# Kernel optimization log

Measured on AMD Instinct MI355X. Metric: run time of the kernel, lower is better.

## Reference

```python
import jax, jax.numpy as jnp
import numpy as np

N_NODE, N_REL, EMB, N_NB, N_TYPES, B = 200000, 16, 128, 16, 4, 4096


def setup_inputs() -> dict:
    key = jax.random.key(0)
    ks = jax.random.split(key, 12)
    s = 1.0 / np.sqrt(EMB)
    return {
        "node": jax.random.randint(ks[0], (B,), 0, N_NODE),
        "relation": jax.random.randint(ks[1], (B,), 0, N_REL),
        "adj_node": jax.random.randint(ks[2], (N_NODE, N_NB), 0, N_NODE),
        "adj_rela": jax.random.randint(ks[3], (N_NODE, N_NB), 0, N_REL),
        "node_type": jax.random.randint(ks[4], (N_NODE,), 0, N_TYPES),
        "node_emb": jax.random.normal(ks[5], (N_NODE, EMB), jnp.float32) * s,
        "rela_emb": jax.random.normal(ks[6], (N_REL, EMB), jnp.float32) * s,
        "type_w": jax.random.uniform(ks[7], (N_TYPES, N_TYPES), jnp.float32),
        "Ws0": jax.random.normal(ks[8], (EMB, EMB), jnp.float32) * s,
        "Wn0": jax.random.normal(ks[9], (EMB, EMB), jnp.float32) * s,
        "Ws1": jax.random.normal(ks[10], (EMB, EMB), jnp.float32) * s,
        "Wn1": jax.random.normal(ks[11], (EMB, EMB), jnp.float32) * s,
    }


def _agg(self_v, nb_v, score, Ws, Wn):
    # self_v: [N,E], nb_v: [N,K,E], score: [N,K] (all neighbors valid -> no mask)
    w = jax.nn.softmax(score, axis=-1)
    agg = jnp.einsum("nk,nke->ne", w, nb_v)
    return self_v @ Ws + agg @ Wn


def reference(node, relation, adj_node, adj_rela, node_type, node_emb, rela_emb,
              type_w, Ws0, Wn0, Ws1, Wn1):
    # --- multi-hop neighbor expansion (get_neighbors) ---
    e1 = adj_node[node]                      # [B,16]
    r1 = adj_rela[node]                      # [B,16]
    e2 = adj_node[e1].reshape(B, -1)         # [B,256]
    r2 = adj_rela[e1].reshape(B, -1)         # [B,256]

    # --- prior embeddings with DistMult-style relation pre-transform ---
    rel_vec = rela_emb[relation]             # [B,E]
    ev0 = node_emb[node] * rel_vec                           # [B,E]
    ev1 = node_emb[e1] * rel_vec[:, None, :]                 # [B,16,E]
    ev2 = node_emb[e2] * rel_vec[:, None, :]                 # [B,256,E]

    # --- relation similarity |cosine| (calc_rsim) ---
    rn = rela_emb / jnp.maximum(jnp.linalg.norm(rela_emb, axis=-1, keepdims=True), 1e-8)
    rsim = jnp.abs(rn @ rn.T)                # [R,R]

    t0 = node_type[node]                     # [B]
    t1 = node_type[e1]                       # [B,16]
    t2 = node_type[e2]                       # [B,256]

    # --- iteration i=0, hop 0 ---
    score00 = rsim[relation[:, None], r1] * type_w[t0[:, None], t1]   # [B,16]
    v0 = jax.nn.relu(_agg(ev0, ev1, score00, Ws0, Wn0))               # [B,E]

    # --- iteration i=0, hop 1 ---
    self1 = ev1.reshape(B * N_NB, EMB)
    nb1 = ev2.reshape(B * N_NB, N_NB, EMB)
    tgt1 = jnp.repeat(relation, N_NB)
    score01 = (rsim[tgt1[:, None], r2.reshape(B * N_NB, N_NB)]
               * type_w[t1.reshape(-1)[:, None], t2.reshape(B * N_NB, N_NB)])
    v1 = jax.nn.relu(_agg(self1, nb1, score01, Ws0, Wn0)).reshape(B, N_NB, EMB)

    # --- iteration i=1, hop 0 (last: no activation) ---
    out = _agg(v0, v1, score00, Ws1, Wn1)    # [B,E]

    # post='none'; norm=1 -> L2 normalize
    out = out / jnp.maximum(jnp.linalg.norm(out, axis=-1, keepdims=True), 1e-12)
    return out
```

## Files before the change

### kernel.cpp

```cpp
#include <hip/hip_runtime.h>
#include <math.h>

#define NB   16
#define EMB  128
#define G    2
#define XSTRIDE 8704

typedef __bf16 bf16x8 __attribute__((ext_vector_type(8)));
typedef __bf16 bf16x4 __attribute__((ext_vector_type(4)));
typedef float  f32x4  __attribute__((ext_vector_type(4)));
typedef int    i32x4  __attribute__((ext_vector_type(4)));

__global__ __launch_bounds__(256) void pack_w_kernel(
    const float* __restrict__ Ws0, const float* __restrict__ Wn0,
    const float* __restrict__ Ws1, const float* __restrict__ Wn1,
    __bf16* __restrict__ pack)
{
    int idx = blockIdx.x * 256 + threadIdx.x;
    if (idx >= 8192) return;
    int l  = idx & 63;
    int nt = (idx >> 6) & 7;
    int s  = (idx >> 9) & 7;
    int m  = idx >> 12;
    int col = nt * 16 + (l & 15);
    int k0  = s * 32 + (l >> 4) * 8;
    const float* Wa = m ? Ws1 : Ws0;
    const float* Wb = m ? Wn1 : Wn0;
    bf16x8 v;
    #pragma unroll
    for (int j = 0; j < 8; ++j) {
        int k = k0 + j;
        float wv = (k < 128) ? Wa[k * EMB + col] : Wb[(k - 128) * EMB + col];
        v[j] = (__bf16)wv;
    }
    *(bf16x8*)(pack + (size_t)idx * 8) = v;
}

__global__ __launch_bounds__(256) void rsim_kernel(
    const float* __restrict__ rela_emb, float* __restrict__ rsim)
{
    __shared__ float dd[16][16];
    int t = threadIdx.x, r = t >> 4, c = t & 15;
    float d = 0.f;
    #pragma unroll
    for (int k4 = 0; k4 < 32; ++k4) {
        f32x4 a = *(const f32x4*)(rela_emb + r * EMB + k4 * 4);
        f32x4 b = *(const f32x4*)(rela_emb + c * EMB + k4 * 4);
        d += a[0]*b[0] + a[1]*b[1] + a[2]*b[2] + a[3]*b[3];
    }
    dd[r][c] = d;
    __syncthreads();
    float nr = fmaxf(sqrtf(dd[r][r]), 1e-8f);
    float nc = fmaxf(sqrtf(dd[c][c]), 1e-8f);
    rsim[t] = fabsf(d) / (nr * nc);
}

__global__ __launch_bounds__(256) void conv_emb_kernel(
    const float* __restrict__ src, __bf16* __restrict__ dst, int n4)
{
    int i = blockIdx.x * 256 + threadIdx.x;
    if (i >= n4) return;
    f32x4 v = ((const f32x4*)src)[i];
    bf16x4 o;
    o[0] = (__bf16)v[0]; o[1] = (__bf16)v[1];
    o[2] = (__bf16)v[2]; o[3] = (__bf16)v[3];
    ((bf16x4*)dst)[i] = o;
}

template<bool BT>
__device__ __forceinline__ f32x4 load_rq(const void* tab, int idx, int q) {
    if constexpr (BT) {
        bf16x4 v = *((const bf16x4*)tab + idx * 32 + q);
        f32x4 r;
        r[0] = (float)v[0]; r[1] = (float)v[1];
        r[2] = (float)v[2]; r[3] = (float)v[3];
        return r;
    } else {
        return *((const f32x4*)tab + idx * 32 + q);
    }
}

template<bool BT>
__global__ __launch_bounds__(256, 4) void gnn_kernel(
    const int* __restrict__ node, const int* __restrict__ relation,
    const int* __restrict__ adj_node, const int* __restrict__ adj_rela,
    const int* __restrict__ node_type, const void* __restrict__ tab,
    const float* __restrict__ rela_emb, const float* __restrict__ type_w,
    const __bf16* __restrict__ packW, const float* __restrict__ rsimg,
    float* __restrict__ out)
{
    __shared__ __align__(16) unsigned char Xb[G * XSTRIDE];
    __shared__ __align__(16) unsigned char Yb[16 * 512];
    __shared__ __align__(16) float scratch[1024];
    __shared__ __align__(16) float sw01[16][16];
    __shared__ __align__(16) int   se2[16][16];
    __shared__ __align__(16) float relv[EMB];
    __shared__ float sw00[G][16];
    __shared__ float srsim[16];
    __shared__ int   se1[16], sr1[16], st1[16];

    const int t  = threadIdx.x;
    const int b0 = blockIdx.x * G;

    {
        f32x4 z = {0.f, 0.f, 0.f, 0.f};
        *(f32x4*)(Yb + t * 16)        = z;
        *(f32x4*)(Yb + 4096 + t * 16) = z;
    }

    for (int e = 0; e < G; ++e) {
        const int nb0 = node[b0 + e];
        const int rel = relation[b0 + e];

        if (t < 16) {
            int e1 = adj_node[nb0 * NB + t];
            se1[t] = e1;
            sr1[t] = adj_rela[nb0 * NB + t];
            st1[t] = node_type[e1];
            srsim[t] = rsimg[rel * 16 + t];
        }
        if (t < EMB) relv[t] = rela_emb[rel * EMB + t];
        __syncthreads();

        {
            int k = t >> 4, j = t & 15;
            int e1k = se1[k];
            int e2  = adj_node[e1k * NB + j];
            int r2  = adj_rela[e1k * NB + j];
            int t2  = node_type[e2];
            se2[k][j] = e2;
            float s = srsim[r2] * type_w[st1[k] * 4 + t2];
            float m = s;
            #pragma unroll
            for (int off = 8; off >= 1; off >>= 1) m = fmaxf(m, __shfl_xor(m, off));
            float ex = __expf(s - m);
            float sum = ex;
            #pragma unroll
            for (int off = 8; off >= 1; off >>= 1) sum += __shfl_xor(sum, off);
            sw01[k][j] = ex / sum;
        }
        {
            int t0type = node_type[nb0];
            if (t < 16) {
                float s = srsim[sr1[t]] * type_w[t0type * 4 + st1[t]];
                float m = s;
                #pragma unroll
                for (int off = 8; off >= 1; off >>= 1) m = fmaxf(m, __shfl_xor(m, off));
                float ex = __expf(s - m);
                float sum = ex;
                #pragma unroll
                for (int off = 8; off >= 1; off >>= 1) sum += __shfl_xor(sum, off);
                sw00[e][t] = ex / sum;
            }
        }
        __syncthreads();

        unsigned char* Xe = Xb + e * XSTRIDE;
        {
            const int q = t & 31;
            const int g = t >> 5;
            const f32x4 rv4 = *(const f32x4*)&relv[q * 4];
            f32x4 pagg = {0.f, 0.f, 0.f, 0.f};

            for (int kx = 0; kx < 2; ++kx) {
                const int k = g + kx * 8;
                const int swz = (k & 7) << 4;

                const f32x4 sv = load_rq<BT>(tab, se1[k], q);
                pagg += sw00[e][k] * sv;
                bf16x4 xs;
                xs[0] = (__bf16)(sv[0] * rv4[0]);
                xs[1] = (__bf16)(sv[1] * rv4[1]);
                xs[2] = (__bf16)(sv[2] * rv4[2]);
                xs[3] = (__bf16)(sv[3] * rv4[3]);
                *(bf16x4*)(Xe + ((k * 512 + q * 8) ^ swz)) = xs;

                i32x4 i0 = *(const i32x4*)&se2[k][0];
                i32x4 i1 = *(const i32x4*)&se2[k][4];
                i32x4 i2 = *(const i32x4*)&se2[k][8];
                i32x4 i3 = *(const i32x4*)&se2[k][12];
                f32x4 w0 = *(const f32x4*)&sw01[k][0];
                f32x4 w1 = *(const f32x4*)&sw01[k][4];
                f32x4 w2 = *(const f32x4*)&sw01[k][8];
                f32x4 w3 = *(const f32x4*)&sw01[k][12];

                f32x4 v0  = load_rq<BT>(tab, i0[0], q);
                f32x4 v1  = load_rq<BT>(tab, i0[1], q);
                f32x4 v2  = load_rq<BT>(tab, i0[2], q);
                f32x4 v3  = load_rq<BT>(tab, i0[3], q);
                f32x4 v4  = load_rq<BT>(tab, i1[0], q);
                f32x4 v5  = load_rq<BT>(tab, i1[1], q);
                f32x4 v6  = load_rq<BT>(tab, i1[2], q);
                f32x4 v7  = load_rq<BT>(tab, i1[3], q);
                f32x4 v8  = load_rq<BT>(tab, i2[0], q);
                f32x4 v9  = load_rq<BT>(tab, i2[1], q);
                f32x4 v10 = load_rq<BT>(tab, i2[2], q);
                f32x4 v11 = load_rq<BT>(tab, i2[3], q);
                f32x4 v12 = load_rq<BT>(tab, i3[0], q);
                f32x4 v13 = load_rq<BT>(tab, i3[1], q);
                f32x4 v14 = load_rq<BT>(tab, i3[2], q);
                f32x4 v15 = load_rq<BT>(tab, i3[3], q);

                f32x4 s01 = w0[0] * v0;  s01 += w0[1] * v1;
                f32x4 s23 = w0[2] * v2;  s23 += w0[3] * v3;
                f32x4 s45 = w1[0] * v4;  s45 += w1[1] * v5;
                f32x4 s67 = w1[2] * v6;  s67 += w1[3] * v7;
                f32x4 s89 = w2[0] * v8;  s89 += w2[1] * v9;
                f32x4 sab = w2[2] * v10; sab += w2[3] * v11;
                f32x4 scd = w3[0] * v12; scd += w3[1] * v13;
                f32x4 sef = w3[2] * v14; sef += w3[3] * v15;
                s01 += s23; s45 += s67; s89 += sab; scd += sef;
                s01 += s45; s89 += scd;
                f32x4 acc = s01 + s89;

                bf16x4 xa;
                xa[0] = (__bf16)(acc[0] * rv4[0]);
                xa[1] = (__bf16)(acc[1] * rv4[1]);
                xa[2] = (__bf16)(acc[2] * rv4[2]);
                xa[3] = (__bf16)(acc[3] * rv4[3]);
                *(bf16x4*)(Xe + ((k * 512 + 256 + q * 8) ^ swz)) = xa;
            }
            ((f32x4*)scratch)[g * 32 + q] = pagg;
        }
        __syncthreads();
        if (t < 32) {
            f32x4 s = ((f32x4*)scratch)[t];
            #pragma unroll
            for (int g = 1; g < 8; ++g) s += ((f32x4*)scratch)[g * 32 + t];
            const f32x4 rv4 = *(const f32x4*)&relv[t * 4];
            const f32x4 ev0 = load_rq<BT>(tab, nb0, t);
            bf16x4 h0s, h0a;
            #pragma unroll
            for (int c = 0; c < 4; ++c) {
                h0s[c] = (__bf16)(ev0[c] * rv4[c]);
                h0a[c] = (__bf16)(s[c]   * rv4[c]);
            }
            *(bf16x4*)(Xe + 16 * 512 + t * 8)       = h0s;
            *(bf16x4*)(Xe + 16 * 512 + 256 + t * 8) = h0a;
        }
        __syncthreads();
    }

    const int w = t >> 6, l = t & 63;
    f32x4 acc[G][2][2];
    #pragma unroll
    for (int e = 0; e < G; ++e)
        #pragma unroll
        for (int m = 0; m < 2; ++m)
            #pragma unroll
            for (int n = 0; n < 2; ++n)
                acc[e][m][n] = (f32x4){0.f, 0.f, 0.f, 0.f};
    {
        const int row0 = l & 15;
        const int kb   = (l >> 4) * 16;
        const int sw0  = (row0 & 7) << 4;
        #pragma unroll
        for (int s = 0; s < 8; ++s) {
            bf16x8 bf0 = *(const bf16x8*)(packW + ((s * 8 + 2 * w) * 64 + l) * 8);
            bf16x8 bf1 = *(const bf16x8*)(packW + ((s * 8 + 2 * w + 1) * 64 + l) * 8);
            #pragma unroll
            for (int e = 0; e < G; ++e) {
                const unsigned char* Xe = Xb + e * XSTRIDE;
                bf16x8 a0 = *(const bf16x8*)(Xe + ((row0 * 512 + s * 64 + kb) ^ sw0));
                bf16x8 a1 = *(const bf16x8*)(Xe + (16 * 512 + s * 64 + kb));
                acc[e][0][0] = __builtin_amdgcn_mfma_f32_16x16x32_bf16(a0, bf0, acc[e][0][0], 0, 0, 0);
                acc[e][0][1] = __builtin_amdgcn_mfma_f32_16x16x32_bf16(a0, bf1, acc[e][0][1], 0, 0, 0);
                acc[e][1][0] = __builtin_amdgcn_mfma_f32_16x16x32_bf16(a1, bf0, acc[e][1][0], 0, 0, 0);
                acc[e][1][1] = __builtin_amdgcn_mfma_f32_16x16x32_bf16(a1, bf1, acc[e][1][1], 0, 0, 0);
            }
        }
    }

    #pragma unroll
    for (int e = 0; e < G; ++e) {
        const int rbase = (l >> 4) * 4;
        float s0 = 0.f, s1 = 0.f;
        #pragma unroll
        for (int r = 0; r < 4; ++r) {
            float wk = sw00[e][rbase + r];
            s0 = fmaf(wk, fmaxf(acc[e][0][0][r], 0.f), s0);
            s1 = fmaf(wk, fmaxf(acc[e][0][1][r], 0.f), s1);
        }
        s0 += __shfl_xor(s0, 16); s0 += __shfl_xor(s0, 32);
        s1 += __shfl_xor(s1, 16); s1 += __shfl_xor(s1, 32);
        if (l < 16) {
            int c0 = 2 * w * 16 + l, c1 = c0 + 16;
            const int swz = (e & 7) << 4;
            *(__bf16*)(Yb + ((e * 512 + c0 * 2) ^ swz))         = (__bf16)fmaxf(acc[e][1][0][0], 0.f);
            *(__bf16*)(Yb + ((e * 512 + c1 * 2) ^ swz))         = (__bf16)fmaxf(acc[e][1][1][0], 0.f);
            *(__bf16*)(Yb + ((e * 512 + (128 + c0) * 2) ^ swz)) = (__bf16)s0;
            *(__bf16*)(Yb + ((e * 512 + (128 + c1) * 2) ^ swz)) = (__bf16)s1;
        }
    }
    __syncthreads();

    {
        f32x4 h0 = {0.f, 0.f, 0.f, 0.f};
        f32x4 h1 = {0.f, 0.f, 0.f, 0.f};
        const int row0 = l & 15;
        const int kb   = (l >> 4) * 16;
        const int sw0  = (row0 & 7) << 4;
        const __bf16* packW1 = packW + 32768;
        #pragma unroll
        for (int s = 0; s < 8; ++s) {
            bf16x8 a   = *(const bf16x8*)(Yb + ((row0 * 512 + s * 64 + kb) ^ sw0));
            bf16x8 bf0 = *(const bf16x8*)(packW1 + ((s * 8 + 2 * w) * 64 + l) * 8);
            bf16x8 bf1 = *(const bf16x8*)(packW1 + ((s * 8 + 2 * w + 1) * 64 + l) * 8);
            h0 = __builtin_amdgcn_mfma_f32_16x16x32_bf16(a, bf0, h0, 0, 0, 0);
            h1 = __builtin_amdgcn_mfma_f32_16x16x32_bf16(a, bf1, h1, 0, 0, 0);
        }
        if (l < 16) {
            int c0 = 2 * w * 16 + l, c1 = c0 + 16;
            #pragma unroll
            for (int e = 0; e < G; ++e) {
                scratch[e * EMB + c0] = h0[e];
                scratch[e * EMB + c1] = h1[e];
            }
        }
    }
    __syncthreads();

    if (t < 64 * G) {
        int e  = t >> 6;
        int c2 = (t & 63) * 2;
        float a  = scratch[e * EMB + c2];
        float bb = scratch[e * EMB + c2 + 1];
        float sq = a * a + bb * bb;
        #pragma unroll
        for (int off = 1; off < 64; off <<= 1) sq += __shfl_xor(sq, off);
        float inv = 1.f / fmaxf(sqrtf(sq), 1e-12f);
        out[(b0 + e) * EMB + c2]     = a * inv;
        out[(b0 + e) * EMB + c2 + 1] = bb * inv;
    }
}

extern "C" void kernel_launch(void* const* d_in, const int* in_sizes, int n_in,
                              void* d_out, int out_size, void* d_ws, size_t ws_size,
                              hipStream_t stream) {
    (void)n_in; (void)out_size;
    const int*   node      = (const int*)d_in[0];
    const int*   relation  = (const int*)d_in[1];
    const int*   adj_node  = (const int*)d_in[2];
    const int*   adj_rela  = (const int*)d_in[3];
    const int*   node_type = (const int*)d_in[4];
    const float* node_emb  = (const float*)d_in[5];
    const float* rela_emb  = (const float*)d_in[6];
    const float* type_w    = (const float*)d_in[7];
    const float* Ws0       = (const float*)d_in[8];
    const float* Wn0       = (const float*)d_in[9];
    const float* Ws1       = (const float*)d_in[10];
    const float* Wn1       = (const float*)d_in[11];
    float* out = (float*)d_out;
    const int B     = in_sizes[0];
    const int nnode = in_sizes[5] / EMB;

    __bf16* packW = (__bf16*)d_ws;
    float*  rsimg = (float*)((char*)d_ws + 131072);
    __bf16* tabbf = (__bf16*)((char*)d_ws + 132096);
    const size_t need = 132096 + (size_t)nnode * EMB * 2;

    pack_w_kernel<<<32, 256, 0, stream>>>(Ws0, Wn0, Ws1, Wn1, packW);
    rsim_kernel<<<1, 256, 0, stream>>>(rela_emb, rsimg);

    const int grid = B / G;
    if (ws_size >= need) {
        const int n4 = nnode * EMB / 4;
        conv_emb_kernel<<<(n4 + 255) / 256, 256, 0, stream>>>(node_emb, tabbf, n4);
        gnn_kernel<true><<<grid, 256, 0, stream>>>(node, relation, adj_node, adj_rela,
                                                   node_type, (const void*)tabbf, rela_emb,
                                                   type_w, packW, rsimg, out);
    } else {
        gnn_kernel<false><<<grid, 256, 0, stream>>>(node, relation, adj_node, adj_rela,
                                                    node_type, (const void*)node_emb, rela_emb,
                                                    type_w, packW, rsimg, out);
    }
}
```

Baseline: 99.11 us.

## Process one batch element per block and reuse one LDS buffer across stages

Changes the gnn kernel from two batch elements per block (G=2) to one, launching B blocks. The Y buffer is dropped: the first-stage X buffer is zeroed and reused for the second-stage MFMA input, and scratch becomes a smaller shared array. The self-embedding row is written earlier by one warp. This cuts LDS use per block and accumulator registers, aiming for higher occupancy and more blocks to hide gather latency. In exchange, each B-fragment load of packW now feeds half as many MFMAs, and the kernel gains an extra barrier.

```diff
diff --git a/kernel.cpp b/kernel.cpp
--- a/kernel.cpp
+++ b/kernel.cpp
@@ -3,8 +3,6 @@
 
 #define NB   16
 #define EMB  128
-#define G    2
-#define XSTRIDE 8704
 
 typedef __bf16 bf16x8 __attribute__((ext_vector_type(8)));
 typedef __bf16 bf16x4 __attribute__((ext_vector_type(4)));
@@ -89,47 +87,51 @@
     const __bf16* __restrict__ packW, const float* __restrict__ rsimg,
     float* __restrict__ out)
 {
-    __shared__ __align__(16) unsigned char Xb[G * XSTRIDE];
-    __shared__ __align__(16) unsigned char Yb[16 * 512];
-    __shared__ __align__(16) float scratch[1024];
+    __shared__ __align__(16) unsigned char Xb[17 * 512];
+    __shared__ __align__(16) f32x4 scr4[8][32];
     __shared__ __align__(16) float sw01[16][16];
     __shared__ __align__(16) int   se2[16][16];
     __shared__ __align__(16) float relv[EMB];
-    __shared__ float sw00[G][16];
+    __shared__ float sw00[16];
     __shared__ float srsim[16];
     __shared__ int   se1[16], sr1[16], st1[16];
 
-    const int t  = threadIdx.x;
-    const int b0 = blockIdx.x * G;
-
-    {
-        f32x4 z = {0.f, 0.f, 0.f, 0.f};
-        *(f32x4*)(Yb + t * 16)        = z;
-        *(f32x4*)(Yb + 4096 + t * 16) = z;
-    }
-
-    for (int e = 0; e < G; ++e) {
-        const int nb0 = node[b0 + e];
-        const int rel = relation[b0 + e];
-
+    const int t   = threadIdx.x;
+    const int b   = blockIdx.x;
+    const int nb0 = node[b];
+    const int rel = relation[b];
+
+    if (t < 16) {
+        int e1 = adj_node[nb0 * NB + t];
+        se1[t] = e1;
+        sr1[t] = adj_rela[nb0 * NB + t];
+        st1[t] = node_type[e1];
+        srsim[t] = rsimg[rel * 16 + t];
+    }
+    if (t < EMB) relv[t] = rela_emb[rel * EMB + t];
+    __syncthreads();
+
+    {
+        int k = t >> 4, j = t & 15;
+        int e1k = se1[k];
+        int e2  = adj_node[e1k * NB + j];
+        int r2  = adj_rela[e1k * NB + j];
+        int t2  = node_type[e2];
+        se2[k][j] = e2;
+        float s = srsim[r2] * type_w[st1[k] * 4 + t2];
+        float m = s;
+        #pragma unroll
+        for (int off = 8; off >= 1; off >>= 1) m = fmaxf(m, __shfl_xor(m, off));
+        float ex = __expf(s - m);
+        float sum = ex;
+        #pragma unroll
+        for (int off = 8; off >= 1; off >>= 1) sum += __shfl_xor(sum, off);
+        sw01[k][j] = ex / sum;
+    }
+    {
+        int t0type = node_type[nb0];
         if (t < 16) {
-            int e1 = adj_node[nb0 * NB + t];
-            se1[t] = e1;
-            sr1[t] = adj_rela[nb0 * NB + t];
-            st1[t] = node_type[e1];
-            srsim[t] = rsimg[rel * 16 + t];
-        }
-        if (t < EMB) relv[t] = rela_emb[rel * EMB + t];
-        __syncthreads();
-
-        {
-            int k = t >> 4, j = t & 15;
-            int e1k = se1[k];
-            int e2  = adj_node[e1k * NB + j];
-            int r2  = adj_rela[e1k * NB + j];
-            int t2  = node_type[e2];
-            se2[k][j] = e2;
-            float s = srsim[r2] * type_w[st1[k] * 4 + t2];
+            float s = srsim[sr1[t]] * type_w[t0type * 4 + st1[t]];
             float m = s;
             #pragma unroll
             for (int off = 8; off >= 1; off >>= 1) m = fmaxf(m, __shfl_xor(m, off));
@@ -137,163 +139,150 @@
             float sum = ex;
             #pragma unroll
             for (int off = 8; off >= 1; off >>= 1) sum += __shfl_xor(sum, off);
-            sw01[k][j] = ex / sum;
-        }
-        {
-            int t0type = node_type[nb0];
-            if (t < 16) {
-                float s = srsim[sr1[t]] * type_w[t0type * 4 + st1[t]];
-                float m = s;
-                #pragma unroll
-                for (int off = 8; off >= 1; off >>= 1) m = fmaxf(m, __shfl_xor(m, off));
-                float ex = __expf(s - m);
-                float sum = ex;
-                #pragma unroll
-                for (int off = 8; off >= 1; off >>= 1) sum += __shfl_xor(sum, off);
-                sw00[e][t] = ex / sum;
-            }
-        }
-        __syncthreads();
-
-        unsigned char* Xe = Xb + e * XSTRIDE;
-        {
-            const int q = t & 31;
-            const int g = t >> 5;
-            const f32x4 rv4 = *(const f32x4*)&relv[q * 4];
-            f32x4 pagg = {0.f, 0.f, 0.f, 0.f};
-
-            for (int kx = 0; kx < 2; ++kx) {
-                const int k = g + kx * 8;
-                const int swz = (k & 7) << 4;
-
-                const f32x4 sv = load_rq<BT>(tab, se1[k], q);
-                pagg += sw00[e][k] * sv;
-                bf16x4 xs;
-                xs[0] = (__bf16)(sv[0] * rv4[0]);
-                xs[1] = (__bf16)(sv[1] * rv4[1]);
-                xs[2] = (__bf16)(sv[2] * rv4[2]);
-                xs[3] = (__bf16)(sv[3] * rv4[3]);
-                *(bf16x4*)(Xe + ((k * 512 + q * 8) ^ swz)) = xs;
-
-                i32x4 i0 = *(const i32x4*)&se2[k][0];
-                i32x4 i1 = *(const i32x4*)&se2[k][4];
-                i32x4 i2 = *(const i32x4*)&se2[k][8];
-                i32x4 i3 = *(const i32x4*)&se2[k][12];
-                f32x4 w0 = *(const f32x4*)&sw01[k][0];
-                f32x4 w1 = *(const f32x4*)&sw01[k][4];
-                f32x4 w2 = *(const f32x4*)&sw01[k][8];
-                f32x4 w3 = *(const f32x4*)&sw01[k][12];
-
-                f32x4 v0  = load_rq<BT>(tab, i0[0], q);
-                f32x4 v1  = load_rq<BT>(tab, i0[1], q);
-                f32x4 v2  = load_rq<BT>(tab, i0[2], q);
-                f32x4 v3  = load_rq<BT>(tab, i0[3], q);
-                f32x4 v4  = load_rq<BT>(tab, i1[0], q);
-                f32x4 v5  = load_rq<BT>(tab, i1[1], q);
-                f32x4 v6  = load_rq<BT>(tab, i1[2], q);
-                f32x4 v7  = load_rq<BT>(tab, i1[3], q);
-                f32x4 v8  = load_rq<BT>(tab, i2[0], q);
-                f32x4 v9  = load_rq<BT>(tab, i2[1], q);
-                f32x4 v10 = load_rq<BT>(tab, i2[2], q);
-                f32x4 v11 = load_rq<BT>(tab, i2[3], q);
-                f32x4 v12 = load_rq<BT>(tab, i3[0], q);
-                f32x4 v13 = load_rq<BT>(tab, i3[1], q);
-                f32x4 v14 = load_rq<BT>(tab, i3[2], q);
-                f32x4 v15 = load_rq<BT>(tab, i3[3], q);
-
-                f32x4 s01 = w0[0] * v0;  s01 += w0[1] * v1;
-                f32x4 s23 = w0[2] * v2;  s23 += w0[3] * v3;
-                f32x4 s45 = w1[0] * v4;  s45 += w1[1] * v5;
-                f32x4 s67 = w1[2] * v6;  s67 += w1[3] * v7;
-                f32x4 s89 = w2[0] * v8;  s89 += w2[1] * v9;
-                f32x4 sab = w2[2] * v10; sab += w2[3] * v11;
-                f32x4 scd = w3[0] * v12; scd += w3[1] * v13;
-                f32x4 sef = w3[2] * v14; sef += w3[3] * v15;
-                s01 += s23; s45 += s67; s89 += sab; scd += sef;
-                s01 += s45; s89 += scd;
-                f32x4 acc = s01 + s89;
-
-                bf16x4 xa;
-                xa[0] = (__bf16)(acc[0] * rv4[0]);
-                xa[1] = (__bf16)(acc[1] * rv4[1]);
-                xa[2] = (__bf16)(acc[2] * rv4[2]);
-                xa[3] = (__bf16)(acc[3] * rv4[3]);
-                *(bf16x4*)(Xe + ((k * 512 + 256 + q * 8) ^ swz)) = xa;
-            }
-            ((f32x4*)scratch)[g * 32 + q] = pagg;
-        }
-        __syncthreads();
-        if (t < 32) {
-            f32x4 s = ((f32x4*)scratch)[t];
+            sw00[t] = ex / sum;
+        }
+    }
+    __syncthreads();
+
+    {
+        const int q = t & 31;
+        const int g = t >> 5;
+        const f32x4 rv4 = *(const f32x4*)&relv[q * 4];
+        f32x4 pagg = {0.f, 0.f, 0.f, 0.f};
+
+        if (g == 0) {
+            const f32x4 ev0 = load_rq<BT>(tab, nb0, q);
+            bf16x4 h0s;
             #pragma unroll
-            for (int g = 1; g < 8; ++g) s += ((f32x4*)scratch)[g * 32 + t];
-            const f32x4 rv4 = *(const f32x4*)&relv[t * 4];
-            const f32x4 ev0 = load_rq<BT>(tab, nb0, t);
-            bf16x4 h0s, h0a;
-            #pragma unroll
-            for (int c = 0; c < 4; ++c) {
-                h0s[c] = (__bf16)(ev0[c] * rv4[c]);
-                h0a[c] = (__bf16)(s[c]   * rv4[c]);
-            }
-            *(bf16x4*)(Xe + 16 * 512 + t * 8)       = h0s;
-            *(bf16x4*)(Xe + 16 * 512 + 256 + t * 8) = h0a;
-        }
-        __syncthreads();
-    }
+            for (int c = 0; c < 4; ++c) h0s[c] = (__bf16)(ev0[c] * rv4[c]);
+            *(bf16x4*)(Xb + 16 * 512 + q * 8) = h0s;
+        }
+
+        for (int kx = 0; kx < 2; ++kx) {
+            const int k = g + kx * 8;
+            const int swz = (k & 7) << 4;
+
+            const f32x4 sv = load_rq<BT>(tab, se1[k], q);
+            pagg += sw00[k] * sv;
+            bf16x4 xs;
+            xs[0] = (__bf16)(sv[0] * rv4[0]);
+            xs[1] = (__bf16)(sv[1] * rv4[1]);
+            xs[2] = (__bf16)(sv[2] * rv4[2]);
+            xs[3] = (__bf16)(sv[3] * rv4[3]);
+            *(bf16x4*)(Xb + ((k * 512 + q * 8) ^ swz)) = xs;
+
+            i32x4 i0 = *(const i32x4*)&se2[k][0];
+            i32x4 i1 = *(const i32x4*)&se2[k][4];
+            i32x4 i2 = *(const i32x4*)&se2[k][8];
+            i32x4 i3 = *(const i32x4*)&se2[k][12];
+            f32x4 w0 = *(const f32x4*)&sw01[k][0];
+            f32x4 w1 = *(const f32x4*)&sw01[k][4];
+            f32x4 w2 = *(const f32x4*)&sw01[k][8];
+            f32x4 w3 = *(const f32x4*)&sw01[k][12];
+
+            f32x4 v0  = load_rq<BT>(tab, i0[0], q);
+            f32x4 v1  = load_rq<BT>(tab, i0[1], q);
+            f32x4 v2  = load_rq<BT>(tab, i0[2], q);
+            f32x4 v3  = load_rq<BT>(tab, i0[3], q);
+            f32x4 v4  = load_rq<BT>(tab, i1[0], q);
+            f32x4 v5  = load_rq<BT>(tab, i1[1], q);
+            f32x4 v6  = load_rq<BT>(tab, i1[2], q);
+            f32x4 v7  = load_rq<BT>(tab, i1[3], q);
+            f32x4 v8  = load_rq<BT>(tab, i2[0], q);
+            f32x4 v9  = load_rq<BT>(tab, i2[1], q);
+            f32x4 v10 = load_rq<BT>(tab, i2[2], q);
+            f32x4 v11 = load_rq<BT>(tab, i2[3], q);
+            f32x4 v12 = load_rq<BT>(tab, i3[0], q);
+            f32x4 v13 = load_rq<BT>(tab, i3[1], q);
+            f32x4 v14 = load_rq<BT>(tab, i3[2], q);
+            f32x4 v15 = load_rq<BT>(tab, i3[3], q);
+
+            f32x4 s01 = w0[0] * v0;  s01 += w0[1] * v1;
+            f32x4 s23 = w0[2] * v2;  s23 += w0[3] * v3;
+            f32x4 s45 = w1[0] * v4;  s45 += w1[1] * v5;
+            f32x4 s67 = w1[2] * v6;  s67 += w1[3] * v7;
+            f32x4 s89 = w2[0] * v8;  s89 += w2[1] * v9;
+            f32x4 sab = w2[2] * v10; sab += w2[3] * v11;
+            f32x4 scd = w3[0] * v12; scd += w3[1] * v13;
+            f32x4 sef = w3[2] * v14; sef += w3[3] * v15;
+            s01 += s23; s45 += s67; s89 += sab; scd += sef;
+            s01 += s45; s89 += scd;
+            f32x4 acc = s01 + s89;
+
+            bf16x4 xa;
+            xa[0] = (__bf16)(acc[0] * rv4[0]);
+            xa[1] = (__bf16)(acc[1] * rv4[1]);
+            xa[2] = (__bf16)(acc[2] * rv4[2]);
+            xa[3] = (__bf16)(acc[3] * rv4[3]);
+            *(bf16x4*)(Xb + ((k * 512 + 256 + q * 8) ^ swz)) = xa;
+        }
+        scr4[g][q] = pagg;
+    }
+    __syncthreads();
+    if (t < 32) {
+        f32x4 s = scr4[0][t];
+        #pragma unroll
+        for (int g = 1; g < 8; ++g) s += scr4[g][t];
+        const f32x4 rv4 = *(const f32x4*)&relv[t * 4];
+        bf16x4 h0a;
+        #pragma unroll
+        for (int c = 0; c < 4; ++c) h0a[c] = (__bf16)(s[c] * rv4[c]);
+        *(bf16x4*)(Xb + 16 * 512 + 256 + t * 8) = h0a;
+    }
+    __syncthreads();
 
     const int w = t >> 6, l = t & 63;
-    f32x4 acc[G][2][2];
-    #pragma unroll
-    for (int e = 0; e < G; ++e)
-        #pragma unroll
-        for (int m = 0; m < 2; ++m)
-            #pragma unroll
-            for (int n = 0; n < 2; ++n)
-                acc[e][m][n] = (f32x4){0.f, 0.f, 0.f, 0.f};
+    f32x4 acc00 = {0.f, 0.f, 0.f, 0.f};
+    f32x4 acc01 = {0.f, 0.f, 0.f, 0.f};
+    f32x4 acc10 = {0.f, 0.f, 0.f, 0.f};
+    f32x4 acc11 = {0.f, 0.f, 0.f, 0.f};
     {
         const int row0 = l & 15;
         const int kb   = (l >> 4) * 16;
         const int sw0  = (row0 & 7) << 4;
         #pragma unroll
         for (int s = 0; s < 8; ++s) {
-            bf16x8 bf0 = *(const bf16x8*)(packW + ((s * 8 + 2 * w) * 64 + l) * 8);
-            bf16x8 bf1 = *(const bf16x8*)(packW + ((s * 8 + 2 * w + 1) * 64 + l) * 8);
-            #pragma unroll
-            for (int e = 0; e < G; ++e) {
-                const unsigned char* Xe = Xb + e * XSTRIDE;
-                bf16x8 a0 = *(const bf16x8*)(Xe + ((row0 * 512 + s * 64 + kb) ^ sw0));
-                bf16x8 a1 = *(const bf16x8*)(Xe + (16 * 512 + s * 64 + kb));
-                acc[e][0][0] = __builtin_amdgcn_mfma_f32_16x16x32_bf16(a0, bf0, acc[e][0][0], 0, 0, 0);
-                acc[e][0][1] = __builtin_amdgcn_mfma_f32_16x16x32_bf16(a0, bf1, acc[e][0][1], 0, 0, 0);
-                acc[e][1][0] = __builtin_amdgcn_mfma_f32_16x16x32_bf16(a1, bf0, acc[e][1][0], 0, 0, 0);
-                acc[e][1][1] = __builtin_amdgcn_mfma_f32_16x16x32_bf16(a1, bf1, acc[e][1][1], 0, 0, 0);
-            }
-        }
-    }
-
-    #pragma unroll
-    for (int e = 0; e < G; ++e) {
+            bf16x8 a0 = *(const bf16x8*)(Xb + ((row0 * 512 + s * 64 + kb) ^ sw0));
+            bf16x8 a1 = *(const bf16x8*)(Xb + (16 * 512 + s * 64 + kb));
+            bf16x8 b0 = *(const bf16x8*)(packW + ((s * 8 + 2 * w) * 64 + l) * 8);
+            bf16x8 b1 = *(const bf16x8*)(packW + ((s * 8 + 2 * w + 1) * 64 + l) * 8);
+            acc00 = __builtin_amdgcn_mfma_f32_16x16x32_bf16(a0, b0, acc00, 0, 0, 0);
+            acc01 = __builtin_amdgcn_mfma_f32_16x16x32_bf16(a0, b1, acc01, 0, 0, 0);
+            acc10 = __builtin_amdgcn_mfma_f32_16x16x32_bf16(a1, b0, acc10, 0, 0, 0);
+            acc11 = __builtin_amdgcn_mfma_f32_16x16x32_bf16(a1, b1, acc11, 0, 0, 0);
+        }
+    }
+    __syncthreads();
+
+    {
+        f32x4 z = {0.f, 0.f, 0.f, 0.f};
+        *(f32x4*)(Xb + t * 32)      = z;
+        *(f32x4*)(Xb + t * 32 + 16) = z;
+    }
+    __syncthreads();
+
+    {
         const int rbase = (l >> 4) * 4;
         float s0 = 0.f, s1 = 0.f;
         #pragma unroll
         for (int r = 0; r < 4; ++r) {
-            float wk = sw00[e][rbase + r];
-            s0 = fmaf(wk, fmaxf(acc[e][0][0][r], 0.f), s0);
-            s1 = fmaf(wk, fmaxf(acc[e][0][1][r], 0.f), s1);
+            float wk = sw00[rbase + r];
+            s0 = fmaf(wk, fmaxf(acc00[r], 0.f), s0);
+            s1 = fmaf(wk, fmaxf(acc01[r], 0.f), s1);
         }
         s0 += __shfl_xor(s0, 16); s0 += __shfl_xor(s0, 32);
         s1 += __shfl_xor(s1, 16); s1 += __shfl_xor(s1, 32);
         if (l < 16) {
             int c0 = 2 * w * 16 + l, c1 = c0 + 16;
-            const int swz = (e & 7) << 4;
-            *(__bf16*)(Yb + ((e * 512 + c0 * 2) ^ swz))         = (__bf16)fmaxf(acc[e][1][0][0], 0.f);
-            *(__bf16*)(Yb + ((e * 512 + c1 * 2) ^ swz))         = (__bf16)fmaxf(acc[e][1][1][0], 0.f);
-            *(__bf16*)(Yb + ((e * 512 + (128 + c0) * 2) ^ swz)) = (__bf16)s0;
-            *(__bf16*)(Yb + ((e * 512 + (128 + c1) * 2) ^ swz)) = (__bf16)s1;
-        }
-    }
-    __syncthreads();
-
+            *(__bf16*)(Xb + c0 * 2)         = (__bf16)fmaxf(acc10[0], 0.f);
+            *(__bf16*)(Xb + c1 * 2)         = (__bf16)fmaxf(acc11[0], 0.f);
+            *(__bf16*)(Xb + (128 + c0) * 2) = (__bf16)s0;
+            *(__bf16*)(Xb + (128 + c1) * 2) = (__bf16)s1;
+        }
+    }
+    __syncthreads();
+
+    float* hout = (float*)scr4;
     {
         f32x4 h0 = {0.f, 0.f, 0.f, 0.f};
         f32x4 h1 = {0.f, 0.f, 0.f, 0.f};
@@ -303,34 +292,29 @@
         const __bf16* packW1 = packW + 32768;
         #pragma unroll
         for (int s = 0; s < 8; ++s) {
-            bf16x8 a   = *(const bf16x8*)(Yb + ((row0 * 512 + s * 64 + kb) ^ sw0));
-            bf16x8 bf0 = *(const bf16x8*)(packW1 + ((s * 8 + 2 * w) * 64 + l) * 8);
-            bf16x8 bf1 = *(const bf16x8*)(packW1 + ((s * 8 + 2 * w + 1) * 64 + l) * 8);
-            h0 = __builtin_amdgcn_mfma_f32_16x16x32_bf16(a, bf0, h0, 0, 0, 0);
-            h1 = __builtin_amdgcn_mfma_f32_16x16x32_bf16(a, bf1, h1, 0, 0, 0);
+            bf16x8 a   = *(const bf16x8*)(Xb + ((row0 * 512 + s * 64 + kb) ^ sw0));
+            bf16x8 b0  = *(const bf16x8*)(packW1 + ((s * 8 + 2 * w) * 64 + l) * 8);
+            bf16x8 b1  = *(const bf16x8*)(packW1 + ((s * 8 + 2 * w + 1) * 64 + l) * 8);
+            h0 = __builtin_amdgcn_mfma_f32_16x16x32_bf16(a, b0, h0, 0, 0, 0);
+            h1 = __builtin_amdgcn_mfma_f32_16x16x32_bf16(a, b1, h1, 0, 0, 0);
         }
         if (l < 16) {
             int c0 = 2 * w * 16 + l, c1 = c0 + 16;
-            #pragma unroll
-            for (int e = 0; e < G; ++e) {
-                scratch[e * EMB + c0] = h0[e];
-                scratch[e * EMB + c1] = h1[e];
-            }
-        }
-    }
-    __syncthreads();
-
-    if (t < 64 * G) {
-        int e  = t >> 6;
-        int c2 = (t & 63) * 2;
-        float a  = scratch[e * EMB + c2];
-        float bb = scratch[e * EMB + c2 + 1];
+            hout[c0] = h0[0];
+            hout[c1] = h1[0];
+        }
+    }
+    __syncthreads();
+
+    if (t < 64) {
+        float a  = hout[t * 2];
+        float bb = hout[t * 2 + 1];
         float sq = a * a + bb * bb;
         #pragma unroll
         for (int off = 1; off < 64; off <<= 1) sq += __shfl_xor(sq, off);
         float inv = 1.f / fmaxf(sqrtf(sq), 1e-12f);
-        out[(b0 + e) * EMB + c2]     = a * inv;
-        out[(b0 + e) * EMB + c2 + 1] = bb * inv;
+        out[b * EMB + t * 2]     = a * inv;
+        out[b * EMB + t * 2 + 1] = bb * inv;
     }
 }
 
@@ -362,16 +346,15 @@
     pack_w_kernel<<<32, 256, 0, stream>>>(Ws0, Wn0, Ws1, Wn1, packW);
     rsim_kernel<<<1, 256, 0, stream>>>(rela_emb, rsimg);
 
-    const int grid = B / G;
     if (ws_size >= need) {
         const int n4 = nnode * EMB / 4;
         conv_emb_kernel<<<(n4 + 255) / 256, 256, 0, stream>>>(node_emb, tabbf, n4);
-        gnn_kernel<true><<<grid, 256, 0, stream>>>(node, relation, adj_node, adj_rela,
-                                                   node_type, (const void*)tabbf, rela_emb,
-                                                   type_w, packW, rsimg, out);
+        gnn_kernel<true><<<B, 256, 0, stream>>>(node, relation, adj_node, adj_rela,
+                                                node_type, (const void*)tabbf, rela_emb,
+                                                type_w, packW, rsimg, out);
     } else {
-        gnn_kernel<false><<<grid, 256, 0, stream>>>(node, relation, adj_node, adj_rela,
-                                                    node_type, (const void*)node_emb, rela_emb,
-                                                    type_w, packW, rsimg, out);
-    }
-}
+        gnn_kernel<false><<<B, 256, 0, stream>>>(node, relation, adj_node, adj_rela,
+                                                 node_type, (const void*)node_emb, rela_emb,
+                                                 type_w, packW, rsimg, out);
+    }
+}
```

Result: no change. 97.70 us (-1.4%).
